# Kernel tuning notes

Hardware: AMD Instinct MI355X
Metric: run time of the kernel (lower is better)

The kernel has to match this reference:

```python
import jax, jax.numpy as jnp
import numpy as np

B, T, S = 64, 256, 512          # batch, decode steps, source length
IN, H, P, C = 512, 512, 256, 512  # in_size, rnn hidden, ctx_proj_size, ctx_size


def setup_inputs() -> dict:
    key = jax.random.key(0)
    ks = jax.random.split(key, 10)
    def n(k, sh, s=0.05):
        return jax.random.normal(k, sh, dtype=jnp.float32) * s
    return {
        "dec_input": n(ks[0], (B, T, IN), 1.0),
        "ctx": n(ks[1], (B, S, C), 1.0),
        "ctx_mask": jnp.ones((B, S), jnp.float32),
        # LSTMCell layer 0: input = in_size + ctx_proj_size (input feeding)
        "Wih0": n(ks[2], (4 * H, IN + P)),
        "Whh0": n(ks[3], (4 * H, H)),
        "bih0": jnp.zeros((4 * H,), jnp.float32),
        "bhh0": jnp.zeros((4 * H,), jnp.float32),
        # LSTMCell layer 1
        "Wih1": n(ks[4], (4 * H, H)),
        "Whh1": n(ks[5], (4 * H, H)),
        "bih1": jnp.zeros((4 * H,), jnp.float32),
        "bhh1": jnp.zeros((4 * H,), jnp.float32),
        # bilinear (Luong general) attention weight
        "Watt": n(ks[6], (H, C)),
        # ctx projection: Linear(rnn_size + att.out_features -> ctx_proj_size)
        "Wproj": n(ks[7], (P, H + C)),
        "bproj": jnp.zeros((P,), jnp.float32),
    }


def _lstm_cell(x, h, c, Wih, Whh, bih, bhh):
    # PyTorch LSTMCell gate order: i, f, g, o
    g = x @ Wih.T + bih + h @ Whh.T + bhh
    i, f, gg, o = jnp.split(g, 4, axis=-1)
    c_new = jax.nn.sigmoid(f) * c + jax.nn.sigmoid(i) * jnp.tanh(gg)
    h_new = jax.nn.sigmoid(o) * jnp.tanh(c_new)
    return h_new, c_new


def reference(dec_input, ctx, ctx_mask, Wih0, Whh0, bih0, bhh0,
              Wih1, Whh1, bih1, bhh1, Watt, Wproj, bproj):
    Bn = dec_input.shape[0]
    neg = (ctx_mask - 1.0) * 1e9  # additive mask: 0 where valid, -1e9 where pad

    def step(carry, x_t):
        h0, c0, h1, c1, feed = carry
        # input feeding at layer 0
        x = jnp.concatenate([x_t, feed], axis=1)
        h0, c0 = _lstm_cell(x, h0, c0, Wih0, Whh0, bih0, bhh0)
        h1, c1 = _lstm_cell(h0, h1, c1, Wih1, Whh1, bih1, bhh1)
        # attention on last layer (att_nth_layer == -1)
        q = h1 @ Watt                                   # [B, C]
        score = jnp.einsum('bc,bsc->bs', q, ctx) + neg  # [B, S]
        alpha = jax.nn.softmax(score, axis=-1)
        ectx = jnp.einsum('bs,bsc->bc', alpha, ctx)     # expected context [B, C]
        # ctx projection with tanh (scale_src = scale_tgt = 1.0)
        res = jnp.tanh(jnp.concatenate([h1, ectx], axis=1) @ Wproj.T + bproj)
        return (h0, c0, h1, c1, res), (res, alpha)

    z = lambda d: jnp.zeros((Bn, d), jnp.float32)
    init = (z(H), z(H), z(H), z(H), z(P))
    _, (dec_out, att_w) = jax.lax.scan(step, init, jnp.swapaxes(dec_input, 0, 1))
    # dec_output [B, T, P], attention weights [B, T, S]
    return jnp.swapaxes(dec_out, 0, 1), jnp.swapaxes(att_w, 0, 1)
```

## Files before the change

### kernel.cpp

```cpp
#include <hip/hip_runtime.h>
#include <math.h>

#define B  64
#define T  256
#define S  512
#define IN 512
#define H  512
#define P  256
#define C  512

typedef _Float16 f16x8 __attribute__((ext_vector_type(8)));
typedef float    f32x4 __attribute__((ext_vector_type(4)));
typedef unsigned short u16x8 __attribute__((ext_vector_type(8)));

#define MFMA16(a, b, c) __builtin_amdgcn_mfma_f32_16x16x32_f16(a, b, c, 0, 0, 0)

#define O_C0      0
#define O_C1      131072
#define O_H0F0    262144
#define O_H1F0    524288
#define O_FEEDF   786432
#define O_H1F32   851968
#define O_XF0     983040
#define O_Q       1245184
#define O_PS      1376256
#define O_PSP     1378304
#define O_PEA     1509376
#define O_BCAT0   2557952
#define O_BCAT1   2566144
#define O_WPROJT  2574336
#define O_W0F     3622912
#define O_PK1A    8865792
#define O_PK1B    9390080
#define O_PK2A    9914368
#define O_PK2B    10438656
#define O_W1F     14108672
#define O_WATTF   22497280
#define O_CTXH    23545856
#define O_H0F1N   57169920
#define O_H1F1N   57300992
#define O_XF1N    57432064

__device__ __forceinline__ float sigm(float x) { return 1.f / (1.f + __expf(-x)); }

__device__ __forceinline__ void split2(float v, unsigned short& hi, unsigned short& lo)
{
    _Float16 h = (_Float16)v;
    float r = (v - (float)h) * 4096.f;
    _Float16 l2 = (_Float16)r;
    union { _Float16 f; unsigned short u; } a, b2;
    a.f = h; b2.f = l2;
    hi = a.u; lo = b2.u;
}

__device__ __forceinline__ unsigned short f2h(float v)
{
    union { _Float16 f; unsigned short u; } x;
    x.f = (_Float16)v;
    return x.u;
}

__device__ __forceinline__ float h2f(unsigned short u)
{
    union { unsigned short u; _Float16 f; } x;
    x.u = u;
    return (float)x.f;
}

__device__ __forceinline__ int frag_us(int r, int k)
{
    return ((((k >> 5) * 4 + (r >> 4)) * 64 + ((k >> 3) & 3) * 16 + (r & 15)) * 16) + (k & 7);
}

__device__ __forceinline__ void gemm_core(
    const unsigned short* A0, int n0, const unsigned short* A1, int n1,
    const unsigned short* A2, const unsigned short* Wf, int wnks, int wbase,
    int nks, int ct, float* red, int tid)
{
    const int l = tid & 63, kh = tid >> 6;
    f32x4 acch[4] = {};
    f32x4 accl[4] = {};
    const int KQ = nks >> 3;
#pragma unroll 2
    for (int i = 0; i < KQ; ++i) {
        const int ks = kh * KQ + i;
        const unsigned short* ap; int ksl;
        if (ks < n0)           { ap = A0; ksl = ks; }
        else if (ks < n0 + n1) { ap = A1; ksl = ks - n0; }
        else                   { ap = A2; ksl = ks - n0 - n1; }
        const f16x8 b = *(const f16x8*)(Wf + ((long)(ct * wnks + wbase + ks) * 64 + l) * 8);
#pragma unroll
        for (int mt = 0; mt < 4; ++mt) {
            const f16x8* app = (const f16x8*)(ap + (((ksl * 4 + mt) * 64 + l) * 16));
            const f16x8 ah = app[0];
            const f16x8 al = app[1];
            acch[mt] = MFMA16(ah, b, acch[mt]);
            accl[mt] = MFMA16(al, b, accl[mt]);
        }
    }
#pragma unroll
    for (int mt = 0; mt < 4; ++mt) {
        f32x4 v = acch[mt] + accl[mt] * (1.f / 4096.f);
        *(f32x4*)&red[(kh * 64 + l) * 20 + mt * 4] = v;
    }
}

__device__ __forceinline__ void part_store(const float* red, float* Pp,
                                           int ct, int tid)
{
    const int b = tid & 63, hl = tid >> 6;
#pragma unroll
    for (int g = 0; g < 4; ++g) {
        const int col = hl * 4 + g;
        const int li  = ((b & 15) >> 2) * 16 + col;
        const int ri  = (b >> 4) * 4 + (b & 3);
        float v = 0.f;
#pragma unroll
        for (int k2 = 0; k2 < 8; ++k2) v += red[(k2 * 64 + li) * 20 + ri];
        Pp[(ct * 16 + col) * 64 + b] = v;
    }
}

__device__ __forceinline__ void lstm_epi_p(const float* red, const float* Pp,
                                           const float* bias, float* cbuf,
                                           unsigned short* hfrag, float* hf32_out,
                                           int ct, int tid)
{
    const int b = tid & 63, hl = tid >> 6;
    float g4[4];
#pragma unroll
    for (int g = 0; g < 4; ++g) {
        const int col = hl * 4 + g;
        const int li  = ((b & 15) >> 2) * 16 + col;
        const int ri  = (b >> 4) * 4 + (b & 3);
        float v = bias[ct * 16 + col] + Pp[(ct * 16 + col) * 64 + b];
#pragma unroll
        for (int k2 = 0; k2 < 8; ++k2) v += red[(k2 * 64 + li) * 20 + ri];
        g4[g] = v;
    }
    const int hg = ct * 4 + hl;
    const float cold = cbuf[b * H + hg];
    const float cn = sigm(g4[1]) * cold + sigm(g4[0]) * tanhf(g4[2]);
    cbuf[b * H + hg] = cn;
    const float hn = sigm(g4[3]) * tanhf(cn);
    unsigned short hi, lo; split2(hn, hi, lo);
    const int fu = frag_us(b, hg);
    hfrag[fu]     = hi;
    hfrag[fu + 8] = lo;
    if (hf32_out) hf32_out[b * H + hg] = hn;
}

__global__ __launch_bounds__(512)
void k1part0_kernel(char* __restrict__ wsb)
{
    __shared__ float lds[10240];
    const int bid = blockIdx.x, tid = threadIdx.x;
    gemm_core((unsigned short*)(wsb + O_XF0), 16,
              (unsigned short*)(wsb + O_H0F0), 16, nullptr,
              (const unsigned short*)(wsb + O_W0F), 40, 0, 32, bid, lds, tid);
    __syncthreads();
    if (tid < 256) part_store(lds, (float*)(wsb + O_PK1A), bid, tid);
}

__global__ __launch_bounds__(512)
void k1fin_kernel(char* __restrict__ wsb, int t)
{
    __shared__ float lds[10240];
    const int bid = blockIdx.x, tid = threadIdx.x;
    const int cur = t & 1, nxt = cur ^ 1;
    unsigned short* h0f[2] = {(unsigned short*)(wsb + O_H0F0), (unsigned short*)(wsb + O_H0F1N)};
    const float* Pk1[2] = {(const float*)(wsb + O_PK1A), (const float*)(wsb + O_PK1B)};

    gemm_core((unsigned short*)(wsb + O_FEEDF), 8, nullptr, 0, nullptr,
              (const unsigned short*)(wsb + O_W0F), 40, 32, 8, bid, lds, tid);
    __syncthreads();
    if (tid < 256)
        lstm_epi_p(lds, Pk1[cur], (const float*)(wsb + O_BCAT0),
                   (float*)(wsb + O_C0), h0f[nxt], nullptr, bid, tid);
}

__global__ __launch_bounds__(512)
void k2fin_kernel(char* __restrict__ wsb, int t)
{
    __shared__ float lds[10240];
    const int bid = blockIdx.x, tid = threadIdx.x;
    const int cur = t & 1, nxt = cur ^ 1;
    unsigned short* h0f[2] = {(unsigned short*)(wsb + O_H0F0), (unsigned short*)(wsb + O_H0F1N)};
    unsigned short* h1f[2] = {(unsigned short*)(wsb + O_H1F0), (unsigned short*)(wsb + O_H1F1N)};
    const float* Pk2[2] = {(const float*)(wsb + O_PK2A), (const float*)(wsb + O_PK2B)};

    gemm_core(h0f[nxt], 16, nullptr, 0, nullptr,
              (const unsigned short*)(wsb + O_W1F), 32, 0, 16, bid, lds, tid);
    __syncthreads();
    if (tid < 256)
        lstm_epi_p(lds, Pk2[cur], (const float*)(wsb + O_BCAT1),
                   (float*)(wsb + O_C1), h1f[nxt], (float*)(wsb + O_H1F32), bid, tid);
}

__global__ __launch_bounds__(512)
void q_kernel(char* __restrict__ wsb, int t)
{
    __shared__ float lds[10240];
    const int bid = blockIdx.x, tid = threadIdx.x;
    const int nxt = (t & 1) ^ 1;
    unsigned short* h1f[2] = {(unsigned short*)(wsb + O_H1F0), (unsigned short*)(wsb + O_H1F1N)};
    float* qbuf = (float*)(wsb + O_Q);

    gemm_core(h1f[nxt], 16, nullptr, 0, nullptr,
              (const unsigned short*)(wsb + O_WATTF), 16, 0, 16, bid, lds, tid);
    __syncthreads();
    if (tid < 256) {
        const int b = tid & 63, cl = tid >> 6;
        float4 vv;
#pragma unroll
        for (int c2 = 0; c2 < 4; ++c2) {
            const int col = cl * 4 + c2;
            const int li  = ((b & 15) >> 2) * 16 + col;
            const int ri  = (b >> 4) * 4 + (b & 3);
            float v = 0.f;
#pragma unroll
            for (int k2 = 0; k2 < 8; ++k2) v += lds[(k2 * 64 + li) * 20 + ri];
            ((float*)&vv)[c2] = v;
        }
        *(float4*)(qbuf + b * C + bid * 16 + cl * 4) = vv;
    }
}

__global__ __launch_bounds__(512)
void attn_parts_kernel(char* __restrict__ wsb, const float* __restrict__ mask, int t)
{
    __shared__ char smem[40960];
    const int bid = blockIdx.x, tid = threadIdx.x;
    const int cur = t & 1, nxt = cur ^ 1;

    if (bid >= 512) {
        if (t + 1 >= T) return;
        float* red = (float*)smem;
        unsigned short* h0f[2] = {(unsigned short*)(wsb + O_H0F0), (unsigned short*)(wsb + O_H0F1N)};
        unsigned short* h1f[2] = {(unsigned short*)(wsb + O_H1F0), (unsigned short*)(wsb + O_H1F1N)};
        unsigned short* xf[2]  = {(unsigned short*)(wsb + O_XF0),  (unsigned short*)(wsb + O_XF1N)};
        if (bid < 640) {
            float* Pk1[2] = {(float*)(wsb + O_PK1A), (float*)(wsb + O_PK1B)};
            gemm_core(xf[nxt], 16, h0f[nxt], 16, nullptr,
                      (const unsigned short*)(wsb + O_W0F), 40, 0, 32, bid - 512, red, tid);
            __syncthreads();
            if (tid < 256) part_store(red, Pk1[nxt], bid - 512, tid);
        } else {
            float* Pk2[2] = {(float*)(wsb + O_PK2A), (float*)(wsb + O_PK2B)};
            gemm_core(h1f[nxt], 16, nullptr, 0, nullptr,
                      (const unsigned short*)(wsb + O_W1F), 32, 16, 16, bid - 640, red, tid);
            __syncthreads();
            if (tid < 256) part_store(red, Pk2[nxt], bid - 640, tid);
        }
        return;
    }

    float* qs = (float*)smem;
    unsigned short* tile = (unsigned short*)(smem + 2048);
    float* scl = (float*)(smem + 35328);

    const int b = bid >> 3, ei = bid & 7;
    const float* qbuf = (const float*)(wsb + O_Q);
    const unsigned short* ctxh = (const unsigned short*)(wsb + O_CTXH);
    float* pS  = (float*)(wsb + O_PSP);
    float* Ps  = (float*)(wsb + O_PS);
    float* Pea = (float*)(wsb + O_PEA);

    const unsigned short* cb16 = ctxh + ((long)b * S + ei * 64) * C;
    u16x8 creg[4];
#pragma unroll
    for (int it = 0; it < 4; ++it)
        creg[it] = *(const u16x8*)(cb16 + (long)(it * 512 + tid) * 8);

    if (tid < 128) ((float4*)qs)[tid] = ((const float4*)(qbuf + (long)b * C))[tid];
    __syncthreads();

    const int row = tid >> 4;
    const int ch  = tid & 15;
    float qv[32];
#pragma unroll
    for (int j = 0; j < 32; ++j) qv[j] = qs[ch * 32 + j];

    float eacc = 0.f;
#pragma unroll
    for (int tt = 0; tt < 2; ++tt) {
#pragma unroll
        for (int it = 0; it < 4; ++it) {
            const int i = it * 512 + tid;
            const int r = (i >> 6) & 31, c8 = i & 63;
            *(u16x8*)&tile[r * 520 + c8 * 8] = creg[it];
        }
        __syncthreads();
        if (tt == 0) {
#pragma unroll
            for (int it = 0; it < 4; ++it)
                creg[it] = *(const u16x8*)(cb16 + 32 * 512 + (long)(it * 512 + tid) * 8);
        }
        float part = 0.f;
#pragma unroll
        for (int j4 = 0; j4 < 4; ++j4) {
            const u16x8 cv = *(const u16x8*)&tile[row * 520 + ch * 32 + j4 * 8];
#pragma unroll
            for (int m = 0; m < 8; ++m)
                part = fmaf(h2f(cv[m]), qv[j4 * 8 + m], part);
        }
        part += __shfl_xor(part, 1);
        part += __shfl_xor(part, 2);
        part += __shfl_xor(part, 4);
        part += __shfl_xor(part, 8);
        if (ch == 0) {
            const int srow = ei * 64 + tt * 32 + row;
            const float sc = part + (mask[(long)b * S + srow] - 1.f) * 1e9f;
            const float p  = __expf(sc - 20.f);
            scl[tt * 32 + row] = p;
            pS[(long)b * S + srow] = p;
        }
        __syncthreads();
#pragma unroll 8
        for (int s = 0; s < 32; ++s)
            eacc = fmaf(scl[tt * 32 + s], h2f(tile[s * 520 + tid]), eacc);
        __syncthreads();
    }

    Pea[(long)bid * 512 + tid] = eacc;
    if (tid < 64) {
        float v = scl[tid];
#pragma unroll
        for (int off = 32; off; off >>= 1) v += __shfl_xor(v, off);
        if (tid == 0) Ps[bid] = v;
    }
}

__global__ __launch_bounds__(512)
void mp_kernel(char* __restrict__ wsb, const float* __restrict__ bproj,
               const float* __restrict__ dec_input, float* __restrict__ out, int t)
{
    __shared__ float ectx[512];
    __shared__ float h1l[512];
    __shared__ float red[512];

    const int bid = blockIdx.x, tid = threadIdx.x;
    const int cur = t & 1;

    if (bid >= 64) {
        if (t + 2 < T) {
            unsigned short* xf[2] = {(unsigned short*)(wsb + O_XF0), (unsigned short*)(wsb + O_XF1N)};
            const int idx = (bid - 64) * 512 + tid;
            const int bb = idx >> 9, k = idx & 511;
            unsigned short hi, lo;
            split2(dec_input[((long)bb * T + (t + 2)) * IN + k], hi, lo);
            unsigned short* dst = xf[cur];
            const int fu = frag_us(bb, k);
            dst[fu]     = hi;
            dst[fu + 8] = lo;
        }
        return;
    }

    const int b = bid;
    const float* Ps  = (const float*)(wsb + O_PS);
    const float* Pea = (const float*)(wsb + O_PEA);
    const float* pS  = (const float*)(wsb + O_PSP);
    const float* h1f32 = (const float*)(wsb + O_H1F32);
    const unsigned short* Wph = (const unsigned short*)(wsb + O_WPROJT);
    unsigned short* feedf = (unsigned short*)(wsb + O_FEEDF);

    float* dec_out = out;
    float* att_out = out + (long)B * T * P;

    float gs = 0.f;
#pragma unroll
    for (int j = 0; j < 8; ++j) gs += Ps[b * 8 + j];
    const float inv = 1.f / gs;

    float v = 0.f;
#pragma unroll
    for (int j = 0; j < 8; ++j) v += Pea[(long)(b * 8 + j) * 512 + tid];
    ectx[tid] = v * inv;
    h1l[tid]  = h1f32[(long)b * H + tid];
    att_out[((long)b * T + t) * S + tid] = pS[(long)b * S + tid] * inv;
    __syncthreads();

    const int p = tid & 255, half = tid >> 8;
    const float* al = half ? ectx : h1l;
    const unsigned short* Wp = Wph + (long)(half * 512) * P + p;
    float acc = 0.f;
#pragma unroll 8
    for (int kk = 0; kk < 512; ++kk)
        acc = fmaf(al[kk], h2f(Wp[(long)kk * P]), acc);
    red[tid] = acc;
    __syncthreads();

    if (tid < 256) {
        float vv = red[tid] + red[tid + 256] + bproj[tid];
        vv = tanhf(vv);
        dec_out[((long)b * T + t) * P + tid] = vv;
        unsigned short hi, lo; split2(vv, hi, lo);
        const int fu = frag_us(b, tid);
        feedf[fu]     = hi;
        feedf[fu + 8] = lo;
    }
}

__global__ __launch_bounds__(256)
void prep_all(const float* __restrict__ dec_input,
              const float* __restrict__ Wih0, const float* __restrict__ Whh0,
              const float* __restrict__ bih0, const float* __restrict__ bhh0,
              const float* __restrict__ Wih1, const float* __restrict__ Whh1,
              const float* __restrict__ bih1, const float* __restrict__ bhh1,
              const float* __restrict__ Watt, const float* __restrict__ Wproj,
              const float* __restrict__ ctx,
              char* __restrict__ wsb)
{
    const int bid = blockIdx.x, tid = threadIdx.x;
    if (bid < 240) {
        float4 z = {0.f, 0.f, 0.f, 0.f};
        ((float4*)wsb)[bid * 256 + tid] = z;
    } else if (bid < 368) {
        const int idx = (bid - 240) * 256 + tid;
        const int bb = idx >> 9, k = idx & 511;
        unsigned short hi, lo;
        split2(dec_input[((long)bb * T) * IN + k], hi, lo);
        unsigned short* xf0 = (unsigned short*)(wsb + O_XF0);
        const int fu = frag_us(bb, k);
        xf0[fu] = hi; xf0[fu + 8] = lo;
    } else if (bid < 384) {
        const int idx = (bid - 368) * 256 + tid;
        if (idx < 2048) {
            const int p = idx, h = p >> 2, g = p & 3, orig = g * H + h;
            ((float*)(wsb + O_BCAT0))[p] = bih0[orig] + bhh0[orig];
        } else {
            const int p = idx - 2048, h = p >> 2, g = p & 3, orig = g * H + h;
            ((float*)(wsb + O_BCAT1))[p] = bih1[orig] + bhh1[orig];
        }
    } else if (bid < 512) {
        const int idx = (bid - 384) * 256 + tid;
        const int n = idx >> 6, k = (idx & 63) * 8;
        u16x8 hv;
#pragma unroll
        for (int j = 0; j < 8; ++j) hv[j] = f2h(Watt[(long)(k + j) * C + n]);
        unsigned short* Wf = (unsigned short*)(wsb + O_WATTF);
        const long base = ((long)((n >> 4) * 16 + (k >> 5)) * 64 + ((k >> 3) & 3) * 16 + (n & 15)) * 8;
        *(u16x8*)(Wf + base) = hv;
    } else if (bid < 1536) {
        const int idx = (bid - 512) * 256 + tid;
        const int k = idx >> 8, p = idx & 255;
        ((unsigned short*)(wsb + O_WPROJT))[k * P + p] = f2h(Wproj[(long)p * (H + C) + k]);
    } else if (bid < 2816) {
        const int idx = (bid - 1536) * 256 + tid;
        const int n = idx / 160, k8 = idx - n * 160;
        const int k = k8 * 8;
        const int h = n >> 2, g = n & 3, orig = g * H + h;
        const float* src;
        if (k < 512)       src = Wih0 + (long)orig * (IN + P) + k;
        else if (k < 1024) src = Whh0 + (long)orig * H + (k - 512);
        else               src = Wih0 + (long)orig * (IN + P) + 512 + (k - 1024);
        u16x8 hv;
#pragma unroll
        for (int j = 0; j < 8; ++j) hv[j] = f2h(src[j]);
        unsigned short* Wf = (unsigned short*)(wsb + O_W0F);
        const long base = ((long)((n >> 4) * 40 + (k >> 5)) * 64 + ((k >> 3) & 3) * 16 + (n & 15)) * 8;
        *(u16x8*)(Wf + base) = hv;
    } else if (bid < 3840) {
        const int idx = (bid - 2816) * 256 + tid;
        const int n = idx >> 7, k = (idx & 127) * 8;
        const int h = n >> 2, g = n & 3, orig = g * H + h;
        const float* src = (k < H) ? (Wih1 + (long)orig * H + k)
                                   : (Whh1 + (long)orig * H + (k - H));
        u16x8 hv;
#pragma unroll
        for (int j = 0; j < 8; ++j) hv[j] = f2h(src[j]);
        unsigned short* Wf = (unsigned short*)(wsb + O_W1F);
        const long base = ((long)((n >> 4) * 32 + (k >> 5)) * 64 + ((k >> 3) & 3) * 16 + (n & 15)) * 8;
        *(u16x8*)(Wf + base) = hv;
    } else if (bid < 7936) {
        const long idx = (long)(bid - 3840) * 256 + tid;
        const float* src = ctx + idx * 16;
        unsigned short* dst = (unsigned short*)(wsb + O_CTXH) + idx * 16;
        u16x8 o0, o1;
#pragma unroll
        for (int j = 0; j < 8; ++j) {
            o0[j] = f2h(src[j]);
            o1[j] = f2h(src[j + 8]);
        }
        *(u16x8*)dst       = o0;
        *(u16x8*)(dst + 8) = o1;
    } else if (bid < 8064) {
        float4 z = {0.f, 0.f, 0.f, 0.f};
        ((float4*)(wsb + O_PK2A))[(bid - 7936) * 256 + tid] = z;
    } else {
        const int idx = (bid - 8064) * 256 + tid;
        const int bb = idx >> 9, k = idx & 511;
        unsigned short hi, lo;
        split2(dec_input[((long)bb * T + 1) * IN + k], hi, lo);
        unsigned short* xf1 = (unsigned short*)(wsb + O_XF1N);
        const int fu = frag_us(bb, k);
        xf1[fu] = hi; xf1[fu + 8] = lo;
    }
}

extern "C" void kernel_launch(void* const* d_in, const int* in_sizes, int n_in,
                              void* d_out, int out_size, void* d_ws, size_t ws_size,
                              hipStream_t stream)
{
    (void)in_sizes; (void)n_in; (void)out_size; (void)ws_size;
    const float* dec_input = (const float*)d_in[0];
    const float* ctx       = (const float*)d_in[1];
    const float* mask      = (const float*)d_in[2];
    const float* Wih0      = (const float*)d_in[3];
    const float* Whh0      = (const float*)d_in[4];
    const float* bih0      = (const float*)d_in[5];
    const float* bhh0      = (const float*)d_in[6];
    const float* Wih1      = (const float*)d_in[7];
    const float* Whh1      = (const float*)d_in[8];
    const float* bih1      = (const float*)d_in[9];
    const float* bhh1      = (const float*)d_in[10];
    const float* Watt      = (const float*)d_in[11];
    const float* Wproj     = (const float*)d_in[12];
    const float* bproj     = (const float*)d_in[13];
    float* out = (float*)d_out;
    char*  wsb = (char*)d_ws;

    prep_all<<<8192, 256, 0, stream>>>(dec_input, Wih0, Whh0, bih0, bhh0,
                                       Wih1, Whh1, bih1, bhh1, Watt, Wproj,
                                       ctx, wsb);
    k1part0_kernel<<<128, 512, 0, stream>>>(wsb);

    for (int t = 0; t < T; ++t) {
        k1fin_kernel<<<128, 512, 0, stream>>>(wsb, t);
        k2fin_kernel<<<128, 512, 0, stream>>>(wsb, t);
        q_kernel<<<32, 512, 0, stream>>>(wsb, t);
        attn_parts_kernel<<<768, 512, 0, stream>>>(wsb, mask, t);
        mp_kernel<<<128, 512, 0, stream>>>(wsb, bproj, dec_input, out, t);
    }
}
```

Before: 13.05 ms.

## Fuse query projection into attention kernel using a global counter spin-wait

Merges the separate q-projection kernel into the attention-parts launch. The first 32 blocks compute q and publish it with atomic stores plus a per-step counter, and the attention blocks spin on that counter before reading q. This removes one kernel launch and its boundary per decode step (256 per run). In exchange it relies on the producer blocks being scheduled before or alongside the spinning consumers, which risks deadlock or stalls, and it adds a small counter-init block to the prep kernel.

```diff
diff --git a/kernel.cpp b/kernel.cpp
--- a/kernel.cpp
+++ b/kernel.cpp
@@ -37,6 +37,7 @@
 #define O_W1F     14108672
 #define O_WATTF   22497280
 #define O_CTXH    23545856
+#define O_CNTA    57100288
 #define O_H0F1N   57169920
 #define O_H1F1N   57300992
 #define O_XF1N    57432064
@@ -198,59 +199,63 @@
 }
 
 __global__ __launch_bounds__(512)
-void q_kernel(char* __restrict__ wsb, int t)
-{
-    __shared__ float lds[10240];
+void attnq_parts_kernel(char* __restrict__ wsb, const float* __restrict__ mask, int t)
+{
+    __shared__ char smem[40960];
     const int bid = blockIdx.x, tid = threadIdx.x;
     const int nxt = (t & 1) ^ 1;
-    unsigned short* h1f[2] = {(unsigned short*)(wsb + O_H1F0), (unsigned short*)(wsb + O_H1F1N)};
+    unsigned* cntq = (unsigned*)(wsb + O_CNTA) + t;
     float* qbuf = (float*)(wsb + O_Q);
 
-    gemm_core(h1f[nxt], 16, nullptr, 0, nullptr,
-              (const unsigned short*)(wsb + O_WATTF), 16, 0, 16, bid, lds, tid);
-    __syncthreads();
-    if (tid < 256) {
-        const int b = tid & 63, cl = tid >> 6;
-        float4 vv;
-#pragma unroll
-        for (int c2 = 0; c2 < 4; ++c2) {
-            const int col = cl * 4 + c2;
-            const int li  = ((b & 15) >> 2) * 16 + col;
-            const int ri  = (b >> 4) * 4 + (b & 3);
-            float v = 0.f;
-#pragma unroll
-            for (int k2 = 0; k2 < 8; ++k2) v += lds[(k2 * 64 + li) * 20 + ri];
-            ((float*)&vv)[c2] = v;
-        }
-        *(float4*)(qbuf + b * C + bid * 16 + cl * 4) = vv;
-    }
-}
-
-__global__ __launch_bounds__(512)
-void attn_parts_kernel(char* __restrict__ wsb, const float* __restrict__ mask, int t)
-{
-    __shared__ char smem[40960];
-    const int bid = blockIdx.x, tid = threadIdx.x;
-    const int cur = t & 1, nxt = cur ^ 1;
-
-    if (bid >= 512) {
+    if (bid < 32) {
+        float* red = (float*)smem;
+        unsigned short* h1f[2] = {(unsigned short*)(wsb + O_H1F0), (unsigned short*)(wsb + O_H1F1N)};
+        gemm_core(h1f[nxt], 16, nullptr, 0, nullptr,
+                  (const unsigned short*)(wsb + O_WATTF), 16, 0, 16, bid, red, tid);
+        __syncthreads();
+        if (tid < 256) {
+            const int b = tid & 63, cl = tid >> 6;
+            float vv[4];
+#pragma unroll
+            for (int c2 = 0; c2 < 4; ++c2) {
+                const int col = cl * 4 + c2;
+                const int li  = ((b & 15) >> 2) * 16 + col;
+                const int ri  = (b >> 4) * 4 + (b & 3);
+                float v = 0.f;
+#pragma unroll
+                for (int k2 = 0; k2 < 8; ++k2) v += red[(k2 * 64 + li) * 20 + ri];
+                vv[c2] = v;
+            }
+            float* qp = qbuf + b * C + bid * 16 + cl * 4;
+            union { float f[2]; unsigned long long u; } p0, p1;
+            p0.f[0] = vv[0]; p0.f[1] = vv[1];
+            p1.f[0] = vv[2]; p1.f[1] = vv[3];
+            atomicExch((unsigned long long*)qp, p0.u);
+            atomicExch(((unsigned long long*)qp) + 1, p1.u);
+        }
+        __syncthreads();
+        if (tid == 0) atomicAdd(cntq, 1u);
+        return;
+    }
+
+    if (bid >= 544) {
         if (t + 1 >= T) return;
         float* red = (float*)smem;
         unsigned short* h0f[2] = {(unsigned short*)(wsb + O_H0F0), (unsigned short*)(wsb + O_H0F1N)};
         unsigned short* h1f[2] = {(unsigned short*)(wsb + O_H1F0), (unsigned short*)(wsb + O_H1F1N)};
         unsigned short* xf[2]  = {(unsigned short*)(wsb + O_XF0),  (unsigned short*)(wsb + O_XF1N)};
-        if (bid < 640) {
+        if (bid < 672) {
             float* Pk1[2] = {(float*)(wsb + O_PK1A), (float*)(wsb + O_PK1B)};
             gemm_core(xf[nxt], 16, h0f[nxt], 16, nullptr,
-                      (const unsigned short*)(wsb + O_W0F), 40, 0, 32, bid - 512, red, tid);
+                      (const unsigned short*)(wsb + O_W0F), 40, 0, 32, bid - 544, red, tid);
             __syncthreads();
-            if (tid < 256) part_store(red, Pk1[nxt], bid - 512, tid);
+            if (tid < 256) part_store(red, Pk1[nxt], bid - 544, tid);
         } else {
             float* Pk2[2] = {(float*)(wsb + O_PK2A), (float*)(wsb + O_PK2B)};
             gemm_core(h1f[nxt], 16, nullptr, 0, nullptr,
-                      (const unsigned short*)(wsb + O_W1F), 32, 16, 16, bid - 640, red, tid);
+                      (const unsigned short*)(wsb + O_W1F), 32, 16, 16, bid - 672, red, tid);
             __syncthreads();
-            if (tid < 256) part_store(red, Pk2[nxt], bid - 640, tid);
+            if (tid < 256) part_store(red, Pk2[nxt], bid - 672, tid);
         }
         return;
     }
@@ -259,8 +264,8 @@
     unsigned short* tile = (unsigned short*)(smem + 2048);
     float* scl = (float*)(smem + 35328);
 
-    const int b = bid >> 3, ei = bid & 7;
-    const float* qbuf = (const float*)(wsb + O_Q);
+    const int aidx = bid - 32;
+    const int b = aidx >> 3, ei = aidx & 7;
     const unsigned short* ctxh = (const unsigned short*)(wsb + O_CTXH);
     float* pS  = (float*)(wsb + O_PSP);
     float* Ps  = (float*)(wsb + O_PS);
@@ -272,6 +277,11 @@
     for (int it = 0; it < 4; ++it)
         creg[it] = *(const u16x8*)(cb16 + (long)(it * 512 + tid) * 8);
 
+    if (tid == 0) {
+        while (__hip_atomic_load(cntq, __ATOMIC_RELAXED, __HIP_MEMORY_SCOPE_AGENT) < 32u)
+            __builtin_amdgcn_s_sleep(2);
+    }
+    __syncthreads();
     if (tid < 128) ((float4*)qs)[tid] = ((const float4*)(qbuf + (long)b * C))[tid];
     __syncthreads();
 
@@ -322,12 +332,12 @@
         __syncthreads();
     }
 
-    Pea[(long)bid * 512 + tid] = eacc;
+    Pea[(long)aidx * 512 + tid] = eacc;
     if (tid < 64) {
         float v = scl[tid];
 #pragma unroll
         for (int off = 32; off; off >>= 1) v += __shfl_xor(v, off);
-        if (tid == 0) Ps[bid] = v;
+        if (tid == 0) Ps[aidx] = v;
     }
 }
 
@@ -488,7 +498,7 @@
     } else if (bid < 8064) {
         float4 z = {0.f, 0.f, 0.f, 0.f};
         ((float4*)(wsb + O_PK2A))[(bid - 7936) * 256 + tid] = z;
-    } else {
+    } else if (bid < 8192) {
         const int idx = (bid - 8064) * 256 + tid;
         const int bb = idx >> 9, k = idx & 511;
         unsigned short hi, lo;
@@ -496,6 +506,8 @@
         unsigned short* xf1 = (unsigned short*)(wsb + O_XF1N);
         const int fu = frag_us(bb, k);
         xf1[fu] = hi; xf1[fu + 8] = lo;
+    } else if (bid == 8192) {
+        ((unsigned*)(wsb + O_CNTA))[tid] = 0u;
     }
 }
 
@@ -521,7 +533,7 @@
     float* out = (float*)d_out;
     char*  wsb = (char*)d_ws;
 
-    prep_all<<<8192, 256, 0, stream>>>(dec_input, Wih0, Whh0, bih0, bhh0,
+    prep_all<<<8193, 256, 0, stream>>>(dec_input, Wih0, Whh0, bih0, bhh0,
                                        Wih1, Whh1, bih1, bhh1, Watt, Wproj,
                                        ctx, wsb);
     k1part0_kernel<<<128, 512, 0, stream>>>(wsb);
@@ -529,8 +541,7 @@
     for (int t = 0; t < T; ++t) {
         k1fin_kernel<<<128, 512, 0, stream>>>(wsb, t);
         k2fin_kernel<<<128, 512, 0, stream>>>(wsb, t);
-        q_kernel<<<32, 512, 0, stream>>>(wsb, t);
-        attn_parts_kernel<<<768, 512, 0, stream>>>(wsb, mask, t);
+        attnq_parts_kernel<<<800, 512, 0, stream>>>(wsb, mask, t);
         mp_kernel<<<128, 512, 0, stream>>>(wsb, bproj, dec_input, out, t);
     }
 }
```

Result: slower. 13.79 ms (+5.6%).
